# Performance work log

Measured on AMD Instinct MI355X. Metric: run time of the kernel, lower is better.

## Reference

```python
import jax, jax.numpy as jnp
import numpy as np

GROUPS = 32
EPS = 1e-6

def group_norm(x, scale, bias):
    B, H, W, C = x.shape
    xg = x.reshape(B, H, W, GROUPS, C // GROUPS)
    mean = xg.mean(axis=(1, 2, 4), keepdims=True)
    var = xg.var(axis=(1, 2, 4), keepdims=True)
    xg = (xg - mean) * jax.lax.rsqrt(var + EPS)
    return xg.reshape(B, H, W, C) * scale + bias

def nin(x, w, b):
    # 1x1 dense over channel dim
    return jnp.einsum('bhwc,cd->bhwd', x, w) + b

def setup_inputs() -> dict:
    key = jax.random.key(0)
    ks = jax.random.split(key, 6)
    B, H, W, C = 8, 64, 64, 256
    s = 1.0 / np.sqrt(C)
    return {
        'x': jax.random.normal(ks[0], (B, H, W, C), jnp.float32),
        'gn_scale': jnp.ones((C,), jnp.float32),
        'gn_bias': jnp.zeros((C,), jnp.float32),
        'Wq': jax.random.normal(ks[1], (C, C), jnp.float32) * s,
        'bq': jnp.zeros((C,), jnp.float32),
        'Wk': jax.random.normal(ks[2], (C, C), jnp.float32) * s,
        'bk': jnp.zeros((C,), jnp.float32),
        'Wv': jax.random.normal(ks[3], (C, C), jnp.float32) * s,
        'bv': jnp.zeros((C,), jnp.float32),
        'Wf': jax.random.normal(ks[4], (C, C), jnp.float32) * s,
        'bf': jnp.zeros((C,), jnp.float32),
    }

def reference(x, gn_scale, gn_bias, Wq, bq, Wk, bk, Wv, bv, Wf, bf):
    B, H, W, C = x.shape
    h = group_norm(x, gn_scale, gn_bias)
    q = nin(h, Wq, bq)
    k = nin(h, Wk, bk)
    v = nin(h, Wv, bv)
    w = jnp.einsum('bhwc,bHWc->bhwHW', q, k) * (C ** -0.5)  # [B,H,W,H,W]
    w = jax.nn.softmax(w.reshape(B, H, W, H * W), axis=-1).reshape(B, H, W, H, W)
    h = jnp.einsum('bhwHW,bHWc->bhwc', w, v)
    h = nin(h, Wf, bf)
    return (x + h) / np.sqrt(2.0)  # skip_rescale=True
```

## Files before the change

### kernel.cpp

```cpp
#include <hip/hip_runtime.h>
#include <math.h>


typedef __attribute__((ext_vector_type(8))) short bf16x8;
typedef __attribute__((ext_vector_type(4))) float f32x4;
typedef __attribute__((ext_vector_type(16))) float f32x16;
typedef unsigned short u16;
typedef unsigned char u8;
typedef __attribute__((address_space(3))) unsigned int lds_u32;
typedef __attribute__((address_space(1))) unsigned int glb_u32;

namespace {
constexpr int Bn = 8;
constexpr int Np = 4096;
constexpr int Cc = 256;
constexpr float kEps = 1e-6f;
constexpr float kRsqrt2 = 0.70710678118654752440f;
constexpr int kRows = Bn * Np;
}

__device__ __forceinline__ u16 f2b(float x) {
  unsigned int u = __float_as_uint(x);
  u += 0x7fffu + ((u >> 16) & 1u);
  return (u16)(u >> 16);
}

__device__ __forceinline__ u8 f2fp8(float x) {
  return (u8)(__builtin_amdgcn_cvt_pk_fp8_f32(x, x, 0, false) & 0xff);
}

__device__ __forceinline__ long lo64(uint4 u) {
  return (long)(((unsigned long)u.y << 32) | (unsigned long)u.x);
}
__device__ __forceinline__ long hi64(uint4 u) {
  return (long)(((unsigned long)u.w << 32) | (unsigned long)u.z);
}

__device__ __forceinline__ void stage16(const void* g, void* l) {
  __builtin_amdgcn_global_load_lds((const glb_u32*)g, (lds_u32*)l, 16, 0, 0);
}

__global__ __launch_bounds__(256) void conv_w_k(
    const float* __restrict__ Wq, const float* __restrict__ Wk,
    const float* __restrict__ Wv, const float* __restrict__ Wf,
    u16* __restrict__ wsw) {
  const int w = blockIdx.x;
  const float* W = (w == 0) ? Wq : (w == 1) ? Wk : (w == 2) ? Wv : Wf;
  const int t = threadIdx.x;
  const int nt = t >> 7, r = t & 127;
  for (int c0 = 0; c0 < 32; ++c0) {
    const int c = blockIdx.y * 32 + c0;
    const float val = W[(size_t)c * Cc + t];
    const int kt = c >> 6, kk = c & 63;
    const size_t byte = (((size_t)(w * 8 + nt * 4 + kt)) << 14) +
                        (((r * 128 + kk * 2)) ^ ((r & 7) << 4));
    *(u16*)((char*)wsw + byte) = f2b(val);
  }
}

__global__ __launch_bounds__(256) void gn_stats_k(const float* __restrict__ x,
                                                  float* __restrict__ st) {
  const int bg = blockIdx.x;
  const int b = bg >> 5, g = bg & 31;
  const float* base = x + (size_t)b * Np * Cc + g * 8;
  float s = 0.f, ss = 0.f;
  for (int i = threadIdx.x; i < Np * 2; i += 256) {
    const int p = i >> 1, hh = (i & 1) * 4;
    const float4 v = *(const float4*)(base + (size_t)p * Cc + hh);
    s += v.x + v.y + v.z + v.w;
    ss += v.x * v.x + v.y * v.y + v.z * v.z + v.w * v.w;
  }
  __shared__ float red[8];
#pragma unroll
  for (int off = 32; off; off >>= 1) {
    s += __shfl_down(s, off);
    ss += __shfl_down(ss, off);
  }
  const int wid = threadIdx.x >> 6;
  if ((threadIdx.x & 63) == 0) { red[wid] = s; red[wid + 4] = ss; }
  __syncthreads();
  if (threadIdx.x == 0) {
    s = red[0] + red[1] + red[2] + red[3];
    ss = red[4] + red[5] + red[6] + red[7];
    const float mean = s * (1.f / 32768.f);
    const float var = ss * (1.f / 32768.f) - mean * mean;
    st[bg * 2] = mean;
    st[bg * 2 + 1] = rsqrtf(var + kEps);
  }
}

__global__ __launch_bounds__(256) void gn_apply_k(const float* __restrict__ x,
                                                  const float* __restrict__ st,
                                                  const float* __restrict__ gs,
                                                  const float* __restrict__ gb,
                                                  u16* __restrict__ hsw) {
  const int total = kRows * Cc / 4;
  for (int i = blockIdx.x * blockDim.x + threadIdx.x; i < total;
       i += gridDim.x * blockDim.x) {
    const int c4 = i & 63;
    const int p = i >> 6;
    const int b = p >> 12;
    const int g = c4 >> 1;
    const float mean = st[(b * 32 + g) * 2];
    const float rstd = st[(b * 32 + g) * 2 + 1];
    const float4 xv = ((const float4*)x)[i];
    const float4 sv = ((const float4*)gs)[c4];
    const float4 bv = ((const float4*)gb)[c4];
    ushort4 o;
    o.x = f2b((xv.x - mean) * rstd * sv.x + bv.x);
    o.y = f2b((xv.y - mean) * rstd * sv.y + bv.y);
    o.z = f2b((xv.z - mean) * rstd * sv.z + bv.z);
    o.w = f2b((xv.w - mean) * rstd * sv.w + bv.w);
    const int mt = p >> 7, r = p & 127;
    const int c = c4 * 4, kt = c >> 6, kk = c & 63;
    const size_t byte = (((size_t)(mt * 4 + kt)) << 14) +
                        (((r * 128 + kk * 2)) ^ ((r & 7) << 4));
    *(ushort4*)((char*)hsw + byte) = o;
  }
}

__global__ __launch_bounds__(256, 2) void gemm_k(
    const u16* __restrict__ A_sw, const u16* __restrict__ wsw,
    const float* __restrict__ bq, const float* __restrict__ bk,
    const float* __restrict__ bv, const float* __restrict__ bf,
    const float* __restrict__ x, u8* __restrict__ qg, u8* __restrict__ kg,
    u8* __restrict__ vtt, float* __restrict__ out, int mode_sel) {
  __shared__ __align__(16) u16 Al[2][8192], Bl[2][8192];
  const int mode = (mode_sel < 0) ? blockIdx.z : mode_sel;
  const int mt0 = blockIdx.x;
  const int nt0 = blockIdx.y;
  const int t = threadIdx.x;
  const int w = t >> 6, l = t & 63;
  const int wm = w >> 1, wn = w & 1;
  const int lr = l & 15, lg = l >> 4;
  f32x4 acc[4][4];
#pragma unroll
  for (int i = 0; i < 4; ++i)
#pragma unroll
    for (int j = 0; j < 4; ++j) acc[i][j] = (f32x4){0.f, 0.f, 0.f, 0.f};

  auto stg = [&](int kt, int nxt) {
    const char* at = (const char*)A_sw + (((size_t)mt0 * 4 + kt) << 14);
    const char* bt =
        (const char*)wsw + (((size_t)(mode * 8 + nt0 * 4 + kt)) << 14);
    char* ad = (char*)&Al[nxt][0];
    char* bd = (char*)&Bl[nxt][0];
#pragma unroll
    for (int p = 0; p < 4; ++p) {
      const int c = p * 256 + t;
      stage16(at + c * 16, ad + c * 16);
      stage16(bt + c * 16, bd + c * 16);
    }
  };

  stg(0, 0);
  __syncthreads();
  for (int kt = 0; kt < 4; ++kt) {
    if (kt < 3) stg(kt + 1, (kt + 1) & 1);
    const char* Ac = (const char*)&Al[kt & 1][0];
    const char* Bc = (const char*)&Bl[kt & 1][0];
    __builtin_amdgcn_s_setprio(1);
#pragma unroll
    for (int ks = 0; ks < 2; ++ks) {
      bf16x8 af[4], bfr[4];
#pragma unroll
      for (int i = 0; i < 4; ++i)
        af[i] = *(const bf16x8*)(
            Ac + (((wm * 64 + i * 16 + lr) * 128 + ks * 64 + lg * 16) ^
                  ((lr & 7) << 4)));
#pragma unroll
      for (int j = 0; j < 4; ++j)
        bfr[j] = *(const bf16x8*)(
            Bc + (((wn * 64 + j * 16 + lr) * 128 + ks * 64 + lg * 16) ^
                  ((lr & 7) << 4)));
#pragma unroll
      for (int i = 0; i < 4; ++i)
#pragma unroll
        for (int j = 0; j < 4; ++j)
          acc[i][j] = __builtin_amdgcn_mfma_f32_16x16x32_bf16(af[i], bfr[j],
                                                              acc[i][j], 0, 0, 0);
    }
    __builtin_amdgcn_s_setprio(0);
    __syncthreads();
  }
  const int m0 = mt0 * 128 + wm * 64;
  const int n0 = nt0 * 128 + wn * 64;
  const float* bias = (mode == 0) ? bq : (mode == 1) ? bk : (mode == 2) ? bv : bf;
  float bv4[4];
#pragma unroll
  for (int j = 0; j < 4; ++j) bv4[j] = bias[n0 + j * 16 + lr];
#pragma unroll
  for (int i = 0; i < 4; ++i)
#pragma unroll
    for (int e = 0; e < 4; ++e) {
      const int m = m0 + i * 16 + lg * 4 + e;
#pragma unroll
      for (int j = 0; j < 4; ++j) {
        const int n = n0 + j * 16 + lr;
        const float val = acc[i][j][e] + bv4[j];
        if (mode == 0) {
          qg[(size_t)m * Cc + n] = f2fp8(val);
        } else if (mode == 1) {
          const size_t pos = ((size_t)(m >> 5)) * 8192 + (n >> 5) * 1024 +
                             ((m & 31) + 32 * ((n >> 3) & 1)) * 16 +
                             ((n >> 4) & 1) * 8 + (n & 7);
          kg[pos] = f2fp8(val);
        } else if (mode == 2) {
          const size_t pos = ((size_t)(m >> 5)) * 8192 + (n >> 5) * 1024 +
                             ((n & 31) + 32 * ((m >> 3) & 1)) * 16 +
                             ((m >> 4) & 1) * 8 + (m & 7);
          vtt[pos] = f2fp8(val);
        } else {
          out[(size_t)m * Cc + n] =
              (x[(size_t)m * Cc + n] + val) * kRsqrt2;
        }
      }
    }
}

__global__ __launch_bounds__(64, 1) void attn_mfma_k(
    const u8* __restrict__ qg, const u8* __restrict__ ksw,
    const u8* __restrict__ vsw, u16* __restrict__ h2) {
  const int id = blockIdx.x;
  const int b = id & 7;
  const int qt = id >> 3;
  const int l = threadIdx.x;
  const int lq = l & 31;
  const int hi = l >> 5;

  const u8* kbase = ksw + (size_t)b * Np * Cc;
  const u8* vbase = vsw + (size_t)b * Np * Cc;

  long qf[16];
  {
    const u8* qrow = qg + ((size_t)b * Np + qt * 32 + lq) * Cc;
#pragma unroll
    for (int i = 0; i < 16; ++i)
      qf[i] = *(const long*)(qrow + i * 16 + hi * 8);
  }
  f32x16 oacc[8];
#pragma unroll
  for (int nb = 0; nb < 8; ++nb)
#pragma unroll
    for (int r = 0; r < 16; ++r) oacc[nb][r] = 0.f;
  float lrow = 0.f;

  auto loadK = [&](int gt, uint4* KR) {
    const u8* kt = kbase + (size_t)gt * 8192;
#pragma unroll
    for (int i = 0; i < 8; ++i) KR[i] = *(const uint4*)(kt + i * 1024 + l * 16);
  };
  auto loadV = [&](int gt, uint4* VR) {
    const u8* vt = vbase + (size_t)gt * 8192;
#pragma unroll
    for (int i = 0; i < 8; ++i) VR[i] = *(const uint4*)(vt + i * 1024 + l * 16);
  };

  auto qk = [&](const uint4* KR, f32x16& s0, f32x16& s1) {
#pragma unroll
    for (int r = 0; r < 16; ++r) { s0[r] = 0.f; s1[r] = 0.f; }
    __builtin_amdgcn_s_setprio(1);
#pragma unroll
    for (int i = 0; i < 8; ++i) {
      const int ip = i >> 1, h = i & 1;
      s0 = __builtin_amdgcn_mfma_f32_32x32x16_fp8_fp8(
          h ? hi64(KR[ip]) : lo64(KR[ip]), qf[2 * ip + h], s0, 0, 0, 0);
      s1 = __builtin_amdgcn_mfma_f32_32x32x16_fp8_fp8(
          h ? hi64(KR[ip + 4]) : lo64(KR[ip + 4]), qf[2 * ip + 8 + h], s1,
          0, 0, 0);
    }
    __builtin_amdgcn_s_setprio(0);
  };

  auto smf = [&](const f32x16& s0, const f32x16& s1, unsigned int* pk,
                 unsigned int* xp) {
    float p_[16];
#pragma unroll
    for (int r = 0; r < 16; ++r)
      p_[r] = __expf((s0[r] + s1[r]) * 0.0625f - 2.0f);
    lrow += ((((p_[0] + p_[1]) + (p_[2] + p_[3])) +
              ((p_[4] + p_[5]) + (p_[6] + p_[7]))) +
             (((p_[8] + p_[9]) + (p_[10] + p_[11])) +
              ((p_[12] + p_[13]) + (p_[14] + p_[15]))));
#pragma unroll
    for (int g = 0; g < 4; ++g) {
      unsigned int r0 = (unsigned int)__builtin_amdgcn_cvt_pk_fp8_f32(
          p_[4 * g + 0], p_[4 * g + 1], 0, false);
      pk[g] = (unsigned int)__builtin_amdgcn_cvt_pk_fp8_f32(
          p_[4 * g + 2], p_[4 * g + 3], (int)r0, true);
      xp[g] = (unsigned int)__shfl_xor((int)pk[g], 32);
    }
  };

  auto qkpv = [&](const uint4* KN, f32x16& s0, f32x16& s1,
                  const unsigned int* pk, const unsigned int* xp,
                  const uint4* VR) {
#pragma unroll
    for (int r = 0; r < 16; ++r) { s0[r] = 0.f; s1[r] = 0.f; }
    const unsigned int la = hi ? xp[hi] : pk[hi];
    const unsigned int ha = hi ? pk[hi] : xp[hi];
    const long pf0 = (long)(((unsigned long)ha << 32) | la);
    const unsigned int lb = hi ? xp[2 + hi] : pk[2 + hi];
    const unsigned int hb = hi ? pk[2 + hi] : xp[2 + hi];
    const long pf1 = (long)(((unsigned long)hb << 32) | lb);
    __builtin_amdgcn_s_setprio(1);
#pragma unroll
    for (int i = 0; i < 8; ++i) {
      const int ip = i >> 1, h = i & 1;
      s0 = __builtin_amdgcn_mfma_f32_32x32x16_fp8_fp8(
          h ? hi64(KN[ip]) : lo64(KN[ip]), qf[2 * ip + h], s0, 0, 0, 0);
      oacc[i] = __builtin_amdgcn_mfma_f32_32x32x16_fp8_fp8(
          lo64(VR[i]), pf0, oacc[i], 0, 0, 0);
      s1 = __builtin_amdgcn_mfma_f32_32x32x16_fp8_fp8(
          h ? hi64(KN[ip + 4]) : lo64(KN[ip + 4]), qf[2 * ip + 8 + h], s1,
          0, 0, 0);
      oacc[(i + 4) & 7] = __builtin_amdgcn_mfma_f32_32x32x16_fp8_fp8(
          hi64(VR[(i + 4) & 7]), pf1, oacc[(i + 4) & 7], 0, 0, 0);
    }
    __builtin_amdgcn_s_setprio(0);
  };

  auto pvf = [&](const unsigned int* pk, const unsigned int* xp,
                 const uint4* VR) {
    __builtin_amdgcn_s_setprio(1);
#pragma unroll
    for (int ks = 0; ks < 2; ++ks) {
      const int g0 = 2 * ks + hi;
      const unsigned int lo32 = hi ? xp[g0] : pk[g0];
      const unsigned int hi32 = hi ? pk[g0] : xp[g0];
      const long pfrag = (long)(((unsigned long)hi32 << 32) | lo32);
#pragma unroll
      for (int nb = 0; nb < 8; ++nb) {
        oacc[nb] = __builtin_amdgcn_mfma_f32_32x32x16_fp8_fp8(
            ks ? hi64(VR[nb]) : lo64(VR[nb]), pfrag, oacc[nb], 0, 0, 0);
      }
    }
    __builtin_amdgcn_s_setprio(0);
  };

  uint4 KA[8], VA[8], KB[8], VB[8];
  f32x16 sA0, sA1, sB0, sB1;
  unsigned int pk[4], xp[4];

  loadK(0, KA); loadV(0, VA);
  loadK(1, KB); loadV(1, VB);
  qk(KA, sA0, sA1);
  for (int jt = 0; jt <= 124; jt += 2) {
    loadK(jt + 2, KA);
    smf(sA0, sA1, pk, xp);
    qkpv(KB, sB0, sB1, pk, xp, VA);
    loadV(jt + 2, VA);
    loadK(jt + 3, KB);
    smf(sB0, sB1, pk, xp);
    qkpv(KA, sA0, sA1, pk, xp, VB);
    loadV(jt + 3, VB);
  }
  smf(sA0, sA1, pk, xp);
  qkpv(KB, sB0, sB1, pk, xp, VA);
  smf(sB0, sB1, pk, xp);
  pvf(pk, xp, VB);

  lrow += __shfl_xor(lrow, 32);
  const float inv = 1.f / lrow;
  const size_t mt = (size_t)b * 32 + (qt >> 2);
  const int r = (qt & 3) * 32 + lq;
#pragma unroll
  for (int nb = 0; nb < 8; ++nb)
#pragma unroll
    for (int g = 0; g < 4; ++g) {
      const int c = nb * 32 + g * 8 + hi * 4;
      const int kt = c >> 6, kk = c & 63;
      ushort4 val;
      val.x = f2b(oacc[nb][4 * g + 0] * inv);
      val.y = f2b(oacc[nb][4 * g + 1] * inv);
      val.z = f2b(oacc[nb][4 * g + 2] * inv);
      val.w = f2b(oacc[nb][4 * g + 3] * inv);
      const size_t byte =
          ((mt * 4 + kt) << 14) + (((r * 128 + kk * 2)) ^ ((r & 7) << 4));
      *(ushort4*)((char*)h2 + byte) = val;
    }
}

extern "C" void kernel_launch(void* const* d_in, const int* in_sizes, int n_in,
                              void* d_out, int out_size, void* d_ws,
                              size_t ws_size, hipStream_t stream) {
  const float* x = (const float*)d_in[0];
  const float* gs = (const float*)d_in[1];
  const float* gb = (const float*)d_in[2];
  const float* Wq = (const float*)d_in[3];
  const float* bq = (const float*)d_in[4];
  const float* Wk = (const float*)d_in[5];
  const float* bk = (const float*)d_in[6];
  const float* Wv = (const float*)d_in[7];
  const float* bv = (const float*)d_in[8];
  const float* Wf = (const float*)d_in[9];
  const float* bf = (const float*)d_in[10];
  float* out = (float*)d_out;

  u16* hsw = (u16*)d_ws;
  u8* qg = (u8*)(hsw + (size_t)kRows * Cc);
  u8* kg = qg + (size_t)kRows * Cc;
  u8* vtt = kg + (size_t)kRows * Cc;
  u16* h2 = (u16*)(vtt + (size_t)kRows * Cc);
  u16* wsw = h2 + (size_t)kRows * Cc;
  float* st = (float*)(wsw + 4 * 8 * 8192);

  conv_w_k<<<dim3(4, 8), dim3(256), 0, stream>>>(Wq, Wk, Wv, Wf, wsw);
  gn_stats_k<<<dim3(Bn * 32), dim3(256), 0, stream>>>(x, st);
  gn_apply_k<<<dim3(1024), dim3(256), 0, stream>>>(x, st, gs, gb, hsw);
  gemm_k<<<dim3(kRows / 128, Cc / 128, 3), dim3(256), 0, stream>>>(
      hsw, wsw, bq, bk, bv, bf, x, qg, kg, vtt, out, -1);
  attn_mfma_k<<<dim3(1024), dim3(64), 0, stream>>>(qg, kg, vtt, h2);
  gemm_k<<<dim3(kRows / 128, Cc / 128, 1), dim3(256), 0, stream>>>(
      h2, wsw, bq, bk, bv, bf, x, qg, kg, vtt, out, 3);
}
```

Baseline: 245.3 us.

## Split attention over two key halves and merge partials in combine kernel

Each attention workgroup now processes only half of the 4096 keys, doubling the grid to 2048 single-wave workgroups. Each writes unnormalized fp32 output partials and row sums to workspace. A new combine kernel adds the two halves, normalizes, and writes the swizzled bf16 layout the final GEMM expects. The aim is more parallelism on a 256-CU device where 1024 single-wave blocks underfill the machine. The cost is roughly 64 MB of extra fp32 partial traffic, one more launch, and a larger workspace. Merging relies on softmax without running-max subtraction (a fixed offset), so both halves share the same scale.

```diff
diff --git a/kernel.cpp b/kernel.cpp
--- a/kernel.cpp
+++ b/kernel.cpp
@@ -218,18 +218,22 @@
     }
 }
 
-__global__ __launch_bounds__(64, 1) void attn_mfma_k(
+__global__ __launch_bounds__(64, 2) void attn_mfma_k(
     const u8* __restrict__ qg, const u8* __restrict__ ksw,
-    const u8* __restrict__ vsw, u16* __restrict__ h2) {
+    const u8* __restrict__ vsw, float* __restrict__ oa,
+    float* __restrict__ ob, float* __restrict__ la, float* __restrict__ lb) {
   const int id = blockIdx.x;
   const int b = id & 7;
-  const int qt = id >> 3;
+  const int qt = (id >> 3) & 127;
+  const int half = id >> 10;
   const int l = threadIdx.x;
   const int lq = l & 31;
   const int hi = l >> 5;
-
-  const u8* kbase = ksw + (size_t)b * Np * Cc;
-  const u8* vbase = vsw + (size_t)b * Np * Cc;
+  float* opart = half ? ob : oa;
+  float* lpart = half ? lb : la;
+
+  const u8* kbase = ksw + (size_t)b * Np * Cc + (size_t)half * 64 * 8192;
+  const u8* vbase = vsw + (size_t)b * Np * Cc + (size_t)half * 64 * 8192;
 
   long qf[16];
   {
@@ -297,12 +301,12 @@
                   const uint4* VR) {
 #pragma unroll
     for (int r = 0; r < 16; ++r) { s0[r] = 0.f; s1[r] = 0.f; }
-    const unsigned int la = hi ? xp[hi] : pk[hi];
-    const unsigned int ha = hi ? pk[hi] : xp[hi];
-    const long pf0 = (long)(((unsigned long)ha << 32) | la);
-    const unsigned int lb = hi ? xp[2 + hi] : pk[2 + hi];
-    const unsigned int hb = hi ? pk[2 + hi] : xp[2 + hi];
-    const long pf1 = (long)(((unsigned long)hb << 32) | lb);
+    const unsigned int la_ = hi ? xp[hi] : pk[hi];
+    const unsigned int ha_ = hi ? pk[hi] : xp[hi];
+    const long pf0 = (long)(((unsigned long)ha_ << 32) | la_);
+    const unsigned int lb_ = hi ? xp[2 + hi] : pk[2 + hi];
+    const unsigned int hb_ = hi ? pk[2 + hi] : xp[2 + hi];
+    const long pf1 = (long)(((unsigned long)hb_ << 32) | lb_);
     __builtin_amdgcn_s_setprio(1);
 #pragma unroll
     for (int i = 0; i < 8; ++i) {
@@ -345,7 +349,7 @@
   loadK(0, KA); loadV(0, VA);
   loadK(1, KB); loadV(1, VB);
   qk(KA, sA0, sA1);
-  for (int jt = 0; jt <= 124; jt += 2) {
+  for (int jt = 0; jt <= 60; jt += 2) {
     loadK(jt + 2, KA);
     smf(sA0, sA1, pk, xp);
     qkpv(KB, sB0, sB1, pk, xp, VA);
@@ -361,24 +365,42 @@
   pvf(pk, xp, VB);
 
   lrow += __shfl_xor(lrow, 32);
-  const float inv = 1.f / lrow;
-  const size_t mt = (size_t)b * 32 + (qt >> 2);
-  const int r = (qt & 3) * 32 + lq;
+  const size_t row = (size_t)b * Np + qt * 32 + lq;
+  if (hi == 0) lpart[row] = lrow;
+  float* orow = opart + row * Cc;
 #pragma unroll
   for (int nb = 0; nb < 8; ++nb)
 #pragma unroll
     for (int g = 0; g < 4; ++g) {
-      const int c = nb * 32 + g * 8 + hi * 4;
-      const int kt = c >> 6, kk = c & 63;
-      ushort4 val;
-      val.x = f2b(oacc[nb][4 * g + 0] * inv);
-      val.y = f2b(oacc[nb][4 * g + 1] * inv);
-      val.z = f2b(oacc[nb][4 * g + 2] * inv);
-      val.w = f2b(oacc[nb][4 * g + 3] * inv);
-      const size_t byte =
-          ((mt * 4 + kt) << 14) + (((r * 128 + kk * 2)) ^ ((r & 7) << 4));
-      *(ushort4*)((char*)h2 + byte) = val;
-    }
+      float4 val;
+      val.x = oacc[nb][4 * g + 0];
+      val.y = oacc[nb][4 * g + 1];
+      val.z = oacc[nb][4 * g + 2];
+      val.w = oacc[nb][4 * g + 3];
+      *(float4*)(orow + nb * 32 + 8 * g + hi * 4) = val;
+    }
+}
+
+__global__ __launch_bounds__(256) void combine_k(
+    const float* __restrict__ oa, const float* __restrict__ ob,
+    const float* __restrict__ la, const float* __restrict__ lb,
+    u16* __restrict__ h2) {
+  const int i = blockIdx.x * 256 + threadIdx.x;
+  const int p = i >> 6;
+  const int c4 = i & 63;
+  const float inv = 1.f / (la[p] + lb[p]);
+  const float4 a = ((const float4*)oa)[i];
+  const float4 bq = ((const float4*)ob)[i];
+  ushort4 o;
+  o.x = f2b((a.x + bq.x) * inv);
+  o.y = f2b((a.y + bq.y) * inv);
+  o.z = f2b((a.z + bq.z) * inv);
+  o.w = f2b((a.w + bq.w) * inv);
+  const int mt = p >> 7, r = p & 127;
+  const int c = c4 * 4, kt = c >> 6, kk = c & 63;
+  const size_t byte = (((size_t)(mt * 4 + kt)) << 14) +
+                      (((r * 128 + kk * 2)) ^ ((r & 7) << 4));
+  *(ushort4*)((char*)h2 + byte) = o;
 }
 
 extern "C" void kernel_launch(void* const* d_in, const int* in_sizes, int n_in,
@@ -404,13 +426,19 @@
   u16* h2 = (u16*)(vtt + (size_t)kRows * Cc);
   u16* wsw = h2 + (size_t)kRows * Cc;
   float* st = (float*)(wsw + 4 * 8 * 8192);
+  float* oa = st + 1024;
+  float* ob = oa + (size_t)kRows * Cc;
+  float* la = ob + (size_t)kRows * Cc;
+  float* lb = la + kRows;
 
   conv_w_k<<<dim3(4, 8), dim3(256), 0, stream>>>(Wq, Wk, Wv, Wf, wsw);
   gn_stats_k<<<dim3(Bn * 32), dim3(256), 0, stream>>>(x, st);
   gn_apply_k<<<dim3(1024), dim3(256), 0, stream>>>(x, st, gs, gb, hsw);
   gemm_k<<<dim3(kRows / 128, Cc / 128, 3), dim3(256), 0, stream>>>(
       hsw, wsw, bq, bk, bv, bf, x, qg, kg, vtt, out, -1);
-  attn_mfma_k<<<dim3(1024), dim3(64), 0, stream>>>(qg, kg, vtt, h2);
+  attn_mfma_k<<<dim3(2048), dim3(64), 0, stream>>>(qg, kg, vtt, oa, ob, la, lb);
+  combine_k<<<dim3(kRows * Cc / 4 / 256), dim3(256), 0, stream>>>(oa, ob, la,
+                                                                  lb, h2);
   gemm_k<<<dim3(kRows / 128, Cc / 128, 1), dim3(256), 0, stream>>>(
       h2, wsw, bq, bk, bv, bf, x, qg, kg, vtt, out, 3);
 }
```

Measured after the change: 673.3 us. +174.4%, slower.
